# Kernel optimization log

Measured on AMD Instinct MI355X. Metric: run time of the kernel, lower is better.

## Reference

```python
import jax, jax.numpy as jnp
import numpy as np
from jax.ops import segment_sum, segment_max

H, C = 2, 32            # heads, per-head channels (hidden = H*C = 64)
HID = H * C
L = 2                   # num_layers
EPS = 1e-5              # LayerNorm eps
NEG_SLOPE = 0.2         # GATv2 leaky_relu slope
NP_, NA_, E_, DIN, DOUT = 200_000, 100_000, 1_000_000, 128, 64


def setup_inputs() -> dict:
    ks = jax.random.split(jax.random.key(0), 16)
    s = 0.05
    return {
        "x_paper": jax.random.normal(ks[0], (NP_, DIN), jnp.float32),
        "x_author": jax.random.normal(ks[1], (NA_, DIN), jnp.float32),
        "ei_writes_src": jax.random.randint(ks[2], (E_,), 0, NA_),
        "ei_writes_dst": jax.random.randint(ks[3], (E_,), 0, NP_),
        "ei_rev_src": jax.random.randint(ks[4], (E_,), 0, NP_),
        "ei_rev_dst": jax.random.randint(ks[5], (E_,), 0, NA_),
        "ei_cites_src": jax.random.randint(ks[6], (E_,), 0, NP_),
        "ei_cites_dst": jax.random.randint(ks[7], (E_,), 0, NP_),
        "inW_paper": jax.random.normal(ks[8], (DIN, HID)) * s,
        "inW_author": jax.random.normal(ks[9], (DIN, HID)) * s,
        "gat_Wl": jax.random.normal(ks[10], (L, 3, HID, HID)) * s,
        "gat_bl": jnp.zeros((L, 3, HID)),
        "gat_Wr": jax.random.normal(ks[11], (L, 3, HID, HID)) * s,
        "gat_br": jnp.zeros((L, 3, HID)),
        "gat_att": jax.random.normal(ks[12], (L, 3, H, C)) * s,
        "gat_bias": jnp.zeros((L, 3, HID)),
        "ln_scale": jnp.ones((L, 2, HID)),
        "ln_bias": jnp.zeros((L, 2, HID)),
        "outW_paper": jax.random.normal(ks[13], (HID, DOUT)) * s,
        "outb_paper": jnp.zeros((DOUT,)),
        "outW_author": jax.random.normal(ks[14], (HID, DOUT)) * s,
        "outb_author": jnp.zeros((DOUT,)),
    }


def _gatv2(h_src, h_dst, src, dst, Wl, bl, Wr, br, att, bias):
    """PyG GATv2Conv(64, 32, heads=2, concat=True, add_self_loops=False)."""
    nd = h_dst.shape[0]
    xl = (h_src @ Wl + bl).reshape(-1, H, C)           # [Ns,H,C]
    xr = (h_dst @ Wr + br).reshape(-1, H, C)           # [Nd,H,C]
    e = jax.nn.leaky_relu(xl[src] + xr[dst], NEG_SLOPE)  # [E,H,C] gather+add
    logits = jnp.einsum('ehc,hc->eh', e, att)          # [E,H]
    m = jax.lax.stop_gradient(segment_max(logits, dst, num_segments=nd))
    ex = jnp.exp(logits - m[dst])                      # stable segment softmax
    den = segment_sum(ex, dst, num_segments=nd)
    alpha = ex / den[dst]                              # [E,H]
    agg = segment_sum(xl[src] * alpha[..., None], dst, num_segments=nd)
    return agg.reshape(nd, HID) + bias


def _ln(v, g, b):
    mu = v.mean(-1, keepdims=True)
    var = ((v - mu) ** 2).mean(-1, keepdims=True)
    return (v - mu) / jnp.sqrt(var + EPS) * g + b


def _forward(x_paper, x_author, ints, params):
    ws, wd, rs, rd, cs, cd = ints
    (inW_p, inW_a, Wl, bl, Wr, br, att, gbias, lng, lnb,
     oWp, obp, oWa, oba) = params
    h = {"paper": x_paper @ inW_p, "author": x_author @ inW_a}
    rels = [("author", "paper", ws, wd),   # writes
            ("paper", "author", rs, rd),   # rev_writes
            ("paper", "paper", cs, cd)]    # cites
    for l in range(L):
        new = {"paper": 0.0, "author": 0.0}
        for r, (st, dt, src, dst) in enumerate(rels):
            new[dt] = new[dt] + _gatv2(h[st], h[dt], src, dst,
                                       Wl[l, r], bl[l, r], Wr[l, r], br[l, r],
                                       att[l, r], gbias[l, r])
        # HeteroConv(aggr='sum') -> LayerNorm -> ReLU (dropout is eval no-op)
        h = {nt: jax.nn.relu(_ln(new[nt], lng[l, i], lnb[l, i]))
             for i, nt in enumerate(("paper", "author"))}
    out_p = h["paper"] @ oWp + obp
    out_a = h["author"] @ oWa + oba
    return jnp.concatenate([out_p, out_a], axis=0)  # [Np+Na, DOUT]


def reference(x_paper, x_author, ei_writes_src, ei_writes_dst, ei_rev_src,
              ei_rev_dst, ei_cites_src, ei_cites_dst, inW_paper, inW_author,
              gat_Wl, gat_bl, gat_Wr, gat_br, gat_att, gat_bias, ln_scale,
              ln_bias, outW_paper, outb_paper, outW_author, outb_author):
    ints = (ei_writes_src, ei_writes_dst, ei_rev_src, ei_rev_dst,
            ei_cites_src, ei_cites_dst)
    params = (inW_paper, inW_author, gat_Wl, gat_bl, gat_Wr, gat_br, gat_att,
              gat_bias, ln_scale, ln_bias, outW_paper, outb_paper,
              outW_author, outb_author)
    return _forward(x_paper, x_author, ints, params)
```

## Files before the change

### kernel.cpp

```cpp
#include <hip/hip_runtime.h>
#include <hip/hip_bf16.h>


#define NPAPER  200000
#define NAUTHOR 100000
#define NEDGE   1000000

#define NB128_P 1563
#define NB128_A 782
#define NB64_P  3125
#define NB64_A  1563

#define BIN_SHIFT 10
#define BIN_SIZE  1024
#define NBIN_P    196
#define NBIN_A    98
#define NBIN_TOT  (NBIN_P + NBIN_A + NBIN_P)
#define CAP_P     8192
#define CAP_A     16384
#define RELOFF1   (NBIN_P * CAP_P)
#define RELOFF2   (NBIN_P * CAP_P + NBIN_A * CAP_A)
#define BINNED_TOT (NBIN_P * CAP_P + NBIN_A * CAP_A + NBIN_P * CAP_P)
#define EPT       8
#define NBLK_BIN  489

#define LOG2E 1.4426950408889634f

typedef __attribute__((ext_vector_type(8))) short short8;
typedef __attribute__((ext_vector_type(4))) float f32x4;
typedef __attribute__((ext_vector_type(2))) float f32x2;

__device__ inline float b2f(__hip_bfloat16 v) { return __bfloat162float(v); }

__device__ inline short f2bs(float f) {
    unsigned u = __float_as_uint(f);
    u += 0x7FFFu + ((u >> 16) & 1u);
    return (short)(u >> 16);
}

__device__ inline float wireF(const void* p, int i, int f32) {
    return f32 ? ((const float*)p)[i]
               : b2f(((const __hip_bfloat16*)p)[i]);
}

__device__ inline const int* sel3(int r, const int* a, const int* b, const int* c) {
    return r == 0 ? a : (r == 1 ? b : c);
}
__device__ inline int* sel3m(int r, int* a, int* b, int* c) {
    return r == 0 ? a : (r == 1 ? b : c);
}

__device__ inline f32x2 unpack2(unsigned u) {
    f32x2 r;
    r.x = __uint_as_float(u << 16);
    r.y = __uint_as_float(u & 0xFFFF0000u);
    return r;
}

template <int CTRL>
__device__ inline float dpp_add(float v) {
    const int r = __builtin_amdgcn_update_dpp(
        0, __float_as_int(v), CTRL, 0xF, 0xF, true);
    return v + __int_as_float(r);
}
__device__ inline float hs16(float v) {
    v = dpp_add<0x128>(v);
    v = dpp_add<0x124>(v);
    v = dpp_add<0x122>(v);
    v = dpp_add<0x121>(v);
    return v;
}
__device__ inline float sum32(float v) {
    v = hs16(v);
    const int s = __builtin_amdgcn_ds_swizzle(__float_as_int(v), 0x401F);
    return v + __int_as_float(s);
}

__global__ void detect_mode(const unsigned* __restrict__ lns, int* __restrict__ flag) {
    if (threadIdx.x == 0 && blockIdx.x == 0)
        flag[0] = (lns[0] == 0x3F800000u) ? 1 : 0;
}

__global__ __launch_bounds__(256) void gemm_in(
    const void* __restrict__ A0v, const void* __restrict__ B0v,
    void* __restrict__ Y0v, int N0, int nt0, int g0,
    const void* __restrict__ A1v, const void* __restrict__ B1v,
    void* __restrict__ Y1v, int N1, int nt1,
    const int* __restrict__ flagp)
{
    const int f32 = flagp[0];
    constexpr int K = 128, SB = K + 8;
    __shared__ short Bs[64 * SB];

    int bid = blockIdx.x;
    const void* Av; const void* Bv; void* Yv; int N, ntiles, gstep, t0;
    if (bid < g0) {
        Av = A0v; Bv = B0v; Yv = Y0v; N = N0; ntiles = nt0; gstep = g0; t0 = bid;
    } else {
        Av = A1v; Bv = B1v; Yv = Y1v; N = N1; ntiles = nt1;
        gstep = (int)gridDim.x - g0; t0 = bid - g0;
    }

    const int tid = threadIdx.x;
    for (int idx = tid; idx < K * 64; idx += 256) {
        const int k = idx >> 6, n = idx & 63;
        const short v = f32 ? f2bs(((const float*)Bv)[idx])
                            : ((const short*)Bv)[idx];
        Bs[n * SB + k] = v;
    }
    __syncthreads();
    if (t0 >= ntiles) return;

    const int wave = tid >> 6;
    const int lane = tid & 63;
    const int l15  = lane & 15;
    const int quad = lane >> 4;

    for (int t = t0; t < ntiles; t += gstep) {
        const int rowbase = t * 64 + wave * 16;
        int r = rowbase + l15;
        if (r >= N) r = N - 1;

        short8 af[4];
#pragma unroll
        for (int kit = 0; kit < 4; kit++) {
            const int k0 = kit * 32 + quad * 8;
            if (f32) {
                const float* Ar = (const float*)Av + (size_t)r * K + k0;
                const float4 x0 = *reinterpret_cast<const float4*>(Ar);
                const float4 x1 = *reinterpret_cast<const float4*>(Ar + 4);
                short8 tt;
                tt[0] = f2bs(x0.x); tt[1] = f2bs(x0.y);
                tt[2] = f2bs(x0.z); tt[3] = f2bs(x0.w);
                tt[4] = f2bs(x1.x); tt[5] = f2bs(x1.y);
                tt[6] = f2bs(x1.z); tt[7] = f2bs(x1.w);
                af[kit] = tt;
            } else {
                af[kit] = *reinterpret_cast<const short8*>(
                    (const short*)Av + (size_t)r * K + k0);
            }
        }

        f32x4 acc[4] = {};
#pragma unroll
        for (int kit = 0; kit < 4; kit++) {
            const int k0 = kit * 32 + quad * 8;
#pragma unroll
            for (int cg = 0; cg < 4; cg++) {
                const short8 bf = *reinterpret_cast<const short8*>(
                    &Bs[(cg * 16 + l15) * SB + k0]);
                acc[cg] = __builtin_amdgcn_mfma_f32_16x16x32_bf16(
                    af[kit], bf, acc[cg], 0, 0, 0);
            }
        }

#pragma unroll
        for (int cg = 0; cg < 4; cg++) {
            const int col = cg * 16 + l15;
#pragma unroll
            for (int rr = 0; rr < 4; rr++) {
                const int row = rowbase + quad * 4 + rr;
                if (row < N)
                    ((__hip_bfloat16*)Yv)[(size_t)row * 64 + col] =
                        __float2bfloat16(acc[cg][rr]);
            }
        }
    }
}

struct J6 {
    const void* A[6];
    const void* W[6];
    int         woff[6];
    const void* bias[6];
    int         boff[6];
    void*       Y[6];
    int         N[6];
    int         nt[6];
    int         gb[7];
};

__global__ __launch_bounds__(256) void gemm_ps6(J6 j, const int* __restrict__ flagp)
{
    const int f32 = flagp[0];
    constexpr int K = 64, SB = K + 8;
    __shared__ short Bs[64 * SB];
    __shared__ float sbias[64];
    __shared__ __align__(16) char outs[4][4096];

    const int bid = blockIdx.x;
    int jid = 0;
#pragma unroll
    for (int q = 0; q < 5; q++)
        if (bid >= j.gb[q + 1]) jid = q + 1;

    const void* Av = j.A[jid];
    void* Yv = j.Y[jid];
    const int N = j.N[jid];
    const int ntiles = j.nt[jid];
    const int gstep = j.gb[jid + 1] - j.gb[jid];
    const int t0 = bid - j.gb[jid];

    const int tid = threadIdx.x;
    {
        const short* Ws = (const short*)j.W[jid];
        const float* Wf = (const float*)j.W[jid];
        const int wo = j.woff[jid];
        for (int idx = tid; idx < K * 64; idx += 256) {
            const int k = idx >> 6, n = idx & 63;
            const short v = f32 ? f2bs(Wf[wo + idx]) : Ws[wo + idx];
            Bs[n * SB + k] = v;
        }
        if (tid < 64)
            sbias[tid] = wireF(j.bias[jid], j.boff[jid] + tid, f32);
    }
    __syncthreads();
    if (t0 >= ntiles) return;

    const int wave = tid >> 6;
    const int lane = tid & 63;
    const int l15  = lane & 15;
    const int quad = lane >> 4;
    char* const myout = outs[wave];

    short8 a_cur[2][2], a_nxt[2][2];

    auto ldA = [&](int t, short8 (&af)[2][2]) {
        const int rowb = t * 128 + wave * 32;
#pragma unroll
        for (int kit = 0; kit < 2; kit++) {
            const int k0 = kit * 32 + quad * 8;
#pragma unroll
            for (int rg = 0; rg < 2; rg++) {
                int r = rowb + rg * 16 + l15;
                if (r >= N) r = N - 1;
                af[kit][rg] = *reinterpret_cast<const short8*>(
                    (const short*)Av + (size_t)r * K + k0);
            }
        }
    };

    ldA(t0, a_cur);
    for (int t = t0; ; ) {
        const int tn = t + gstep;
        const bool hn = tn < ntiles;
        if (hn) ldA(tn, a_nxt);

        f32x4 acc[2][4] = {};
#pragma unroll
        for (int kit = 0; kit < 2; kit++) {
            const int k0 = kit * 32 + quad * 8;
#pragma unroll
            for (int cg = 0; cg < 4; cg++) {
                const short8 bf = *reinterpret_cast<const short8*>(
                    &Bs[(cg * 16 + l15) * SB + k0]);
#pragma unroll
                for (int rg = 0; rg < 2; rg++)
                    acc[rg][cg] = __builtin_amdgcn_mfma_f32_16x16x32_bf16(
                        a_cur[kit][rg], bf, acc[rg][cg], 0, 0, 0);
            }
        }

        const int rowbase = t * 128 + wave * 32;
#pragma unroll
        for (int rg = 0; rg < 2; rg++)
#pragma unroll
        for (int cg = 0; cg < 4; cg++) {
            const int col = cg * 16 + l15;
            const float bv = sbias[col];
#pragma unroll
            for (int r = 0; r < 4; r++) {
                const int rl = rg * 16 + quad * 4 + r;
                const unsigned a = (unsigned)(rl * 128 + col * 2)
                                 ^ (unsigned)((rl & 7) << 4);
                *reinterpret_cast<short*>(myout + a) =
                    f2bs(acc[rg][cg][r] + bv);
            }
        }
#pragma unroll
        for (int i = 0; i < 4; i++) {
            const unsigned a = i * 1024 + lane * 16;
            const int rl = a >> 7;
            const unsigned as = a ^ (unsigned)((rl & 7) << 4);
            const int grow = rowbase + rl;
            if (grow < N) {
                const uint4 v = *reinterpret_cast<const uint4*>(myout + as);
                *reinterpret_cast<uint4*>(
                    (__hip_bfloat16*)Yv + (size_t)grow * 64 + ((a & 127) >> 1)) = v;
            }
        }

        if (!hn) break;
#pragma unroll
        for (int kit = 0; kit < 2; kit++) {
            a_cur[kit][0] = a_nxt[kit][0];
            a_cur[kit][1] = a_nxt[kit][1];
        }
        t = tn;
    }
}

__global__ __launch_bounds__(256) void gemm_out(
    const void* __restrict__ A0v, const void* __restrict__ B0v,
    const void* __restrict__ bias0v,
    void* __restrict__ Yv, int N0, int row0_off, int nt0, int g0,
    const void* __restrict__ A1v, const void* __restrict__ B1v,
    const void* __restrict__ bias1v, int N1, int row1_off, int nt1,
    const int* __restrict__ flagp)
{
    const int f32 = flagp[0];
    constexpr int K = 64, SB = K + 8;
    __shared__ short Bs[64 * SB];
    __shared__ float sbias[64];
    __shared__ __align__(16) char outs[4][8192];

    int bid = blockIdx.x;
    const void* Av; const void* Bv; const void* biasv;
    int N, row_off, ntiles, gstep, t0;
    if (bid < g0) {
        Av = A0v; Bv = B0v; biasv = bias0v; N = N0; row_off = row0_off;
        ntiles = nt0; gstep = g0; t0 = bid;
    } else {
        Av = A1v; Bv = B1v; biasv = bias1v; N = N1; row_off = row1_off;
        ntiles = nt1; gstep = (int)gridDim.x - g0; t0 = bid - g0;
    }

    const int tid = threadIdx.x;
    for (int idx = tid; idx < K * 64; idx += 256) {
        const int k = idx >> 6, n = idx & 63;
        const short v = f32 ? f2bs(((const float*)Bv)[idx])
                            : ((const short*)Bv)[idx];
        Bs[n * SB + k] = v;
    }
    if (tid < 64) sbias[tid] = wireF(biasv, tid, f32);
    __syncthreads();
    if (t0 >= ntiles) return;

    const int wave = tid >> 6;
    const int lane = tid & 63;
    const int l15  = lane & 15;
    const int quad = lane >> 4;
    char* const myout = outs[wave];

    short8 a_cur[2][2], a_nxt[2][2];
    auto ldA = [&](int t, short8 (&af)[2][2]) {
        const int rowb = t * 128 + wave * 32;
#pragma unroll
        for (int kit = 0; kit < 2; kit++) {
            const int k0 = kit * 32 + quad * 8;
#pragma unroll
            for (int rg = 0; rg < 2; rg++) {
                int r = rowb + rg * 16 + l15;
                if (r >= N) r = N - 1;
                af[kit][rg] = *reinterpret_cast<const short8*>(
                    (const short*)Av + (size_t)r * K + k0);
            }
        }
    };

    ldA(t0, a_cur);
    for (int t = t0; ; ) {
        const int tn = t + gstep;
        const bool hn = tn < ntiles;
        if (hn) ldA(tn, a_nxt);

        f32x4 acc[2][4] = {};
#pragma unroll
        for (int kit = 0; kit < 2; kit++) {
            const int k0 = kit * 32 + quad * 8;
#pragma unroll
            for (int cg = 0; cg < 4; cg++) {
                const short8 bf = *reinterpret_cast<const short8*>(
                    &Bs[(cg * 16 + l15) * SB + k0]);
#pragma unroll
                for (int rg = 0; rg < 2; rg++)
                    acc[rg][cg] = __builtin_amdgcn_mfma_f32_16x16x32_bf16(
                        a_cur[kit][rg], bf, acc[rg][cg], 0, 0, 0);
            }
        }

        const int rowbase = t * 128 + wave * 32;
        if (!f32) {
#pragma unroll
            for (int rg = 0; rg < 2; rg++)
#pragma unroll
            for (int cg = 0; cg < 4; cg++) {
                const int col = cg * 16 + l15;
                const float bv = sbias[col];
#pragma unroll
                for (int r = 0; r < 4; r++) {
                    const int rl = rg * 16 + quad * 4 + r;
                    const unsigned a = (unsigned)(rl * 128 + col * 2)
                                     ^ (unsigned)((rl & 7) << 4);
                    *reinterpret_cast<short*>(myout + a) =
                        f2bs(acc[rg][cg][r] + bv);
                }
            }
#pragma unroll
            for (int i = 0; i < 4; i++) {
                const unsigned a = i * 1024 + lane * 16;
                const int rl = a >> 7;
                const unsigned as = a ^ (unsigned)((rl & 7) << 4);
                const int grow = rowbase + rl;
                if (grow < N) {
                    const uint4 v = *reinterpret_cast<const uint4*>(myout + as);
                    *reinterpret_cast<uint4*>(
                        (__hip_bfloat16*)Yv
                        + (size_t)(grow + row_off) * 64 + ((a & 127) >> 1)) = v;
                }
            }
        } else {
#pragma unroll
            for (int rg = 0; rg < 2; rg++)
#pragma unroll
            for (int cg = 0; cg < 4; cg++) {
                const int col = cg * 16 + l15;
                const float bv = sbias[col];
#pragma unroll
                for (int r = 0; r < 4; r++) {
                    const int rl = rg * 16 + quad * 4 + r;
                    const unsigned a = (unsigned)(rl * 256 + col * 4)
                                     ^ (unsigned)((rl & 15) << 4);
                    *reinterpret_cast<float*>(myout + a) = acc[rg][cg][r] + bv;
                }
            }
#pragma unroll
            for (int i = 0; i < 8; i++) {
                const unsigned a = i * 1024 + lane * 16;
                const int rl = a >> 8;
                const unsigned as = a ^ (unsigned)((rl & 15) << 4);
                const int grow = rowbase + rl;
                if (grow < N) {
                    const float4 v = *reinterpret_cast<const float4*>(myout + as);
                    *reinterpret_cast<float4*>(
                        (float*)Yv
                        + (size_t)(grow + row_off) * 64 + ((a & 255) >> 2)) = v;
                }
            }
        }

        if (!hn) break;
#pragma unroll
        for (int kit = 0; kit < 2; kit++) {
            a_cur[kit][0] = a_nxt[kit][0];
            a_cur[kit][1] = a_nxt[kit][1];
        }
        t = tn;
    }
}

__global__ __launch_bounds__(256) void scatter_pad(
    const int* __restrict__ s0, const int* __restrict__ s1, const int* __restrict__ s2,
    const int* __restrict__ d0, const int* __restrict__ d1, const int* __restrict__ d2,
    int* __restrict__ g_bincnt, unsigned* __restrict__ binned)
{
    int bid = blockIdx.x;
    const int rel = bid / NBLK_BIN;
    bid -= rel * NBLK_BIN;
    const int* src = sel3(rel, s0, s1, s2);
    const int* dst = sel3(rel, d0, d1, d2);
    const int nbin = (rel == 1) ? NBIN_A : NBIN_P;
    const int cap  = (rel == 1) ? CAP_A : CAP_P;
    const int boff = (rel == 0) ? 0 : ((rel == 1) ? NBIN_P : NBIN_P + NBIN_A);
    unsigned* bout = binned + ((rel == 0) ? 0 : ((rel == 1) ? RELOFF1 : RELOFF2));

    __shared__ int lcnt[NBIN_P];
    __shared__ int lbase[NBIN_P];
    for (int i = threadIdx.x; i < nbin; i += 256) lcnt[i] = 0;
    __syncthreads();

    const int e0 = bid * (256 * EPT) + threadIdx.x;
    int mybin[EPT], myslot[EPT];
    unsigned mypack[EPT];
#pragma unroll
    for (int i = 0; i < EPT; i++) {
        const int e = e0 + i * 256;
        if (e < NEDGE) {
            const int D = dst[e];
            const int b = D >> BIN_SHIFT;
            mybin[i]  = b;
            mypack[i] = (unsigned)src[e] | ((unsigned)(D & (BIN_SIZE - 1)) << 18);
            myslot[i] = atomicAdd(&lcnt[b], 1);
        } else mybin[i] = -1;
    }
    __syncthreads();
    for (int i = threadIdx.x; i < nbin; i += 256) {
        const int cn = lcnt[i];
        lbase[i] = cn ? atomicAdd(&g_bincnt[boff + i], cn) : 0;
    }
    __syncthreads();
#pragma unroll
    for (int i = 0; i < EPT; i++)
        if (mybin[i] >= 0) {
            const int pos = lbase[mybin[i]] + myslot[i];
            if (pos < cap)
                bout[(size_t)mybin[i] * cap + pos] = mypack[i];
        }
}

__global__ __launch_bounds__(256) void csr_binscan(
    const int* __restrict__ g_bincnt, int* __restrict__ g_binbase,
    int* __restrict__ rp0, int* __restrict__ rp1, int* __restrict__ rp2)
{
    __shared__ int lds[NBIN_TOT];
    for (int i = threadIdx.x; i < NBIN_TOT; i += 256) lds[i] = g_bincnt[i];
    __syncthreads();
    if (threadIdx.x < 3) {
        const int rel  = threadIdx.x;
        const int nbin = (rel == 1) ? NBIN_A : NBIN_P;
        const int boff = (rel == 0) ? 0 : ((rel == 1) ? NBIN_P : NBIN_P + NBIN_A);
        int run = 0;
        for (int i = 0; i < nbin; i++) {
            const int cn = lds[boff + i];
            lds[boff + i] = run;
            run += cn;
        }
        int* rp = sel3m(rel, rp0, rp1, rp2);
        rp[(rel == 1) ? NAUTHOR : NPAPER] = NEDGE;
    }
    __syncthreads();
    for (int i = threadIdx.x; i < NBIN_TOT; i += 256)
        g_binbase[i] = lds[i];
}

__global__ __launch_bounds__(256) void csr_build(
    const unsigned* __restrict__ binned, const int* __restrict__ g_binbase,
    const int* __restrict__ g_bincnt,
    int* __restrict__ rp0, int* __restrict__ rp1, int* __restrict__ rp2,
    int* __restrict__ c0, int* __restrict__ c1, int* __restrict__ c2)
{
    int bid = blockIdx.x;
    int rel, boff, N, cap;
    const unsigned* bin;
    if (bid < NBIN_P) {
        rel = 0; boff = 0; N = NPAPER; cap = CAP_P;
        bin = binned + (size_t)bid * CAP_P;
    } else if (bid < NBIN_P + NBIN_A) {
        rel = 1; bid -= NBIN_P; boff = NBIN_P; N = NAUTHOR; cap = CAP_A;
        bin = binned + RELOFF1 + (size_t)bid * CAP_A;
    } else {
        rel = 2; bid -= NBIN_P + NBIN_A; boff = NBIN_P + NBIN_A; N = NPAPER; cap = CAP_P;
        bin = binned + RELOFF2 + (size_t)bid * CAP_P;
    }

    const int base = g_binbase[boff + bid];
    int cnt = g_bincnt[boff + bid];
    if (cnt > cap) cnt = cap;
    int* row_ptr = sel3m(rel, rp0, rp1, rp2);
    int* csr     = sel3m(rel, c0, c1, c2);

    __shared__ int off[BIN_SIZE];
    __shared__ int lds[256];
    for (int i = threadIdx.x; i < BIN_SIZE; i += 256) off[i] = 0;
    __syncthreads();
    for (int i = threadIdx.x; i < cnt; i += 256)
        atomicAdd(&off[bin[i] >> 18], 1);
    __syncthreads();

    const int t  = threadIdx.x;
    const int i4 = t * 4;
    const int v0 = off[i4], v1 = off[i4 + 1], v2 = off[i4 + 2], v3 = off[i4 + 3];
    const int tsum = v0 + v1 + v2 + v3;
    lds[t] = tsum;
    __syncthreads();
    for (int o = 1; o < 256; o <<= 1) {
        const int x = (t >= o) ? lds[t - o] : 0;
        __syncthreads();
        lds[t] += x;
        __syncthreads();
    }
    const int run = lds[t] - tsum;
    const int ex0 = run, ex1 = ex0 + v0, ex2 = ex1 + v1, ex3 = ex2 + v2;
    off[i4] = ex0; off[i4 + 1] = ex1; off[i4 + 2] = ex2; off[i4 + 3] = ex3;
    const int d0g = bid * BIN_SIZE + i4;
    if (d0g     < N) row_ptr[d0g]     = base + ex0;
    if (d0g + 1 < N) row_ptr[d0g + 1] = base + ex1;
    if (d0g + 2 < N) row_ptr[d0g + 2] = base + ex2;
    if (d0g + 3 < N) row_ptr[d0g + 3] = base + ex3;
    __syncthreads();

    for (int i = threadIdx.x; i < cnt; i += 256) {
        const unsigned pk = bin[i];
        const int slot = atomicAdd(&off[pk >> 18], 1);
        csr[base + slot] = (int)(pk & 0x3FFFFu);
    }
}

__device__ inline void gat_core_h(
    const int* __restrict__ csr_src, const unsigned* __restrict__ xlw,
    int beg, int end, int hbase, int cp,
    const f32x2 xr2, float a0, float a1,
    float& accx, float& accy, float& den)
{
    const int n = end - beg;
    const int m = (n + 3) >> 2;
    f32x2 acc2 = {0.0f, 0.0f};
    float dn = 0.0f;

    int lidx;
    {
        const int e = beg + cp;
        lidx = csr_src[(e < end) ? e : beg];
    }
    auto loadq = [&](unsigned (&B)[4], int it) {
#pragma unroll
        for (int k = 0; k < 4; k++) {
            const int s = __shfl(lidx, hbase + ((it & 7) << 2) + k, 64);
            B[k] = xlw[(size_t)s * 32 + cp];
        }
    };

    unsigned G[4];
    loadq(G, 0);
    for (int it = 0; ; ) {
        const int nx = it + 1;
        const bool hn = nx < m;
        unsigned H[4];
        if (hn) {
            if ((nx & 7) == 0) {
                const int e = beg + (nx << 2) + cp;
                lidx = csr_src[(e < end) ? e : beg];
            }
            loadq(H, nx);
        }

        f32x2 xv[4];
        float u[4];
#pragma unroll
        for (int k = 0; k < 4; k++) {
            xv[k] = unpack2(G[k]);
            f32x2 t = xv[k] + xr2;
            t = __builtin_elementwise_max(t, 0.2f * t);
            u[k] = fmaf(t.y, a1, t.x * a0);
        }
#pragma unroll
        for (int k = 0; k < 4; k++) u[k] = hs16(u[k]);
#pragma unroll
        for (int k = 0; k < 4; k++) {
            const float e = ((it << 2) + k < n)
                          ? __builtin_amdgcn_exp2f(u[k]) : 0.0f;
            acc2 += e * xv[k];
            dn   += e;
        }

        if (!hn) break;
        G[0] = H[0]; G[1] = H[1]; G[2] = H[2]; G[3] = H[3];
        it = nx;
    }
    accx = acc2.x;
    accy = acc2.y;
    den  = dn;
}

__global__ __launch_bounds__(256) void gat_all(
    const int* __restrict__ rp0, const int* __restrict__ cs0,
    const __hip_bfloat16* __restrict__ xl0, const __hip_bfloat16* __restrict__ xr0,
    const int* __restrict__ rp2, const int* __restrict__ cs2,
    const __hip_bfloat16* __restrict__ xl2, const __hip_bfloat16* __restrict__ xr2,
    const int* __restrict__ rp1, const int* __restrict__ cs1,
    const __hip_bfloat16* __restrict__ xl1, const __hip_bfloat16* __restrict__ xr1,
    const void* __restrict__ att, int ao0, int ao1, int ao2,
    const void* __restrict__ gb, int bo0, int bo1, int bo2,
    const void* __restrict__ lng, int goffP, int goffA,
    const void* __restrict__ lnb, int boffP, int boffA,
    __hip_bfloat16* __restrict__ h_p, __hip_bfloat16* __restrict__ h_a,
    const int* __restrict__ flagp)
{
    const int gnode = blockIdx.x * 8 + (threadIdx.x >> 5);
    const int hbase = threadIdx.x & 32;
    const int cp    = threadIdx.x & 31;
    const int f32   = flagp[0];
    const int c0 = 2 * cp, c1 = 2 * cp + 1;

    float vx, vy;
    int goff, boff;
    __hip_bfloat16* hout; int dout;

    if (gnode < NPAPER) {
        const int d = gnode;
        vx = wireF(gb, bo0 + c0, f32) + wireF(gb, bo2 + c0, f32);
        vy = wireF(gb, bo0 + c1, f32) + wireF(gb, bo2 + c1, f32);

        {
            const int beg = rp0[d], end = rp0[d + 1];
            if (beg != end) {
                const unsigned uxr = ((const unsigned*)xr0)[(size_t)d * 32 + cp];
                float ax, ay, dn;
                gat_core_h(cs0, (const unsigned*)xl0, beg, end, hbase, cp,
                           unpack2(uxr),
                           wireF(att, ao0 + c0, f32) * LOG2E,
                           wireF(att, ao0 + c1, f32) * LOG2E, ax, ay, dn);
                vx += ax / dn; vy += ay / dn;
            }
        }
        {
            const int beg = rp2[d], end = rp2[d + 1];
            if (beg != end) {
                const unsigned uxr = ((const unsigned*)xr2)[(size_t)d * 32 + cp];
                float ax, ay, dn;
                gat_core_h(cs2, (const unsigned*)xl2, beg, end, hbase, cp,
                           unpack2(uxr),
                           wireF(att, ao2 + c0, f32) * LOG2E,
                           wireF(att, ao2 + c1, f32) * LOG2E, ax, ay, dn);
                vx += ax / dn; vy += ay / dn;
            }
        }
        goff = goffP; boff = boffP;
        hout = h_p; dout = d;
    } else {
        const int d = gnode - NPAPER;
        if (d >= NAUTHOR) return;
        vx = wireF(gb, bo1 + c0, f32);
        vy = wireF(gb, bo1 + c1, f32);

        const int beg = rp1[d], end = rp1[d + 1];
        if (beg != end) {
            const unsigned uxr = ((const unsigned*)xr1)[(size_t)d * 32 + cp];
            float ax, ay, dn;
            gat_core_h(cs1, (const unsigned*)xl1, beg, end, hbase, cp,
                       unpack2(uxr),
                       wireF(att, ao1 + c0, f32) * LOG2E,
                       wireF(att, ao1 + c1, f32) * LOG2E, ax, ay, dn);
            vx += ax / dn; vy += ay / dn;
        }
        goff = goffA; boff = boffA;
        hout = h_a; dout = d;
    }

    const float mu = sum32(vx + vy) * (1.0f / 64.0f);
    const float dx = vx - mu, dy = vy - mu;
    const float var = sum32(dx * dx + dy * dy) * (1.0f / 64.0f);
    const float sc = rsqrtf(var + 1e-5f);
    float y0 = dx * sc * wireF(lng, goff + c0, f32) + wireF(lnb, boff + c0, f32);
    float y1 = dy * sc * wireF(lng, goff + c1, f32) + wireF(lnb, boff + c1, f32);
    y0 = (y0 < 0.0f) ? 0.0f : y0;
    y1 = (y1 < 0.0f) ? 0.0f : y1;

    const unsigned u = (unsigned)(unsigned short)f2bs(y0)
                     | ((unsigned)(unsigned short)f2bs(y1) << 16);
    ((unsigned*)hout)[(size_t)dout * 32 + cp] = u;
}

extern "C" void kernel_launch(void* const* d_in, const int* in_sizes, int n_in,
                              void* d_out, int out_size, void* d_ws, size_t ws_size,
                              hipStream_t stream)
{
    const void* x_p   = d_in[0];
    const void* x_a   = d_in[1];
    const int* e_ws_s = (const int*)d_in[2];
    const int* e_ws_d = (const int*)d_in[3];
    const int* e_rv_s = (const int*)d_in[4];
    const int* e_rv_d = (const int*)d_in[5];
    const int* e_ci_s = (const int*)d_in[6];
    const int* e_ci_d = (const int*)d_in[7];
    const void* inW_p = d_in[8];
    const void* inW_a = d_in[9];
    const void* Wl    = d_in[10];
    const void* bl    = d_in[11];
    const void* Wr    = d_in[12];
    const void* br    = d_in[13];
    const void* att   = d_in[14];
    const void* gbias = d_in[15];
    const void* lng   = d_in[16];
    const void* lnb   = d_in[17];
    const void* oWp   = d_in[18];
    const void* obp   = d_in[19];
    const void* oWa   = d_in[20];
    const void* oba   = d_in[21];

    char* p = (char*)d_ws;
    auto carve = [&](size_t bytes) -> char* {
        char* r = p;
        p += (bytes + 255) & ~(size_t)255;
        return r;
    };
    int* flag = (int*)carve(256);
    __hip_bfloat16* h_p = (__hip_bfloat16*)carve((size_t)NPAPER  * 64 * 2);
    __hip_bfloat16* h_a = (__hip_bfloat16*)carve((size_t)NAUTHOR * 64 * 2);
    __hip_bfloat16* xl0 = (__hip_bfloat16*)carve((size_t)NAUTHOR * 64 * 2);
    __hip_bfloat16* xr0 = (__hip_bfloat16*)carve((size_t)NPAPER  * 64 * 2);
    __hip_bfloat16* xl1 = (__hip_bfloat16*)carve((size_t)NPAPER  * 64 * 2);
    __hip_bfloat16* xr1 = (__hip_bfloat16*)carve((size_t)NAUTHOR * 64 * 2);
    __hip_bfloat16* xl2 = (__hip_bfloat16*)carve((size_t)NPAPER  * 64 * 2);
    __hip_bfloat16* xr2 = (__hip_bfloat16*)carve((size_t)NPAPER  * 64 * 2);
    int *csr_src[3], *row_ptr[3];
    for (int r = 0; r < 3; r++) {
        csr_src[r] = (int*)carve((size_t)NEDGE * 4);
        row_ptr[r] = (int*)carve(((size_t)NPAPER + 1) * 4);
    }
    unsigned* binned = (unsigned*)carve((size_t)BINNED_TOT * 4);
    int* g_bincnt  = (int*)carve(NBIN_TOT * 4);
    int* g_binbase = (int*)carve(NBIN_TOT * 4);

    detect_mode<<<dim3(1), dim3(64), 0, stream>>>((const unsigned*)lng, flag);

    (void)hipMemsetAsync(g_bincnt, 0, NBIN_TOT * 4, stream);
    scatter_pad<<<dim3(3 * NBLK_BIN), dim3(256), 0, stream>>>(
        e_ws_s, e_rv_s, e_ci_s, e_ws_d, e_rv_d, e_ci_d, g_bincnt, binned);
    csr_binscan<<<dim3(1), dim3(256), 0, stream>>>(
        g_bincnt, g_binbase, row_ptr[0], row_ptr[1], row_ptr[2]);
    csr_build<<<dim3(NBIN_TOT), dim3(256), 0, stream>>>(
        binned, g_binbase, g_bincnt, row_ptr[0], row_ptr[1], row_ptr[2],
        csr_src[0], csr_src[1], csr_src[2]);

    {
        const int GT = 2048;
        const int g0 = (int)((long long)GT * NB64_P / (NB64_P + NB64_A));
        gemm_in<<<dim3(GT), dim3(256), 0, stream>>>(
            x_p, inW_p, h_p, NPAPER, NB64_P, g0,
            x_a, inW_a, h_a, NAUTHOR, NB64_A, flag);
    }

    for (int l = 0; l < 2; l++) {
        const int wo0 = (l * 3 + 0) * 4096, bo0 = (l * 3 + 0) * 64;
        const int wo1 = (l * 3 + 1) * 4096, bo1 = (l * 3 + 1) * 64;
        const int wo2 = (l * 3 + 2) * 4096, bo2 = (l * 3 + 2) * 64;

        J6 j;
        const void* As[6] = { h_a, h_p, h_p, h_p, h_p, h_a };
        const void* Ws[6] = { Wl,  Wr,  Wl,  Wr,  Wl,  Wr  };
        const int  wos[6] = { wo0, wo0, wo2, wo2, wo1, wo1 };
        const void* Bi[6] = { bl,  br,  bl,  br,  bl,  br  };
        const int  bos[6] = { bo0, bo0, bo2, bo2, bo1, bo1 };
        void*      Ys[6] = { xl0, xr0, xl2, xr2, xl1, xr1 };
        const int  Nsz[6] = { NAUTHOR, NPAPER, NPAPER, NPAPER, NPAPER, NAUTHOR };
        const int  nts[6] = { NB128_A, NB128_P, NB128_P, NB128_P, NB128_P, NB128_A };
        const int GT6 = 1536;
        int total = 0;
        for (int q = 0; q < 6; q++) total += nts[q];
        j.gb[0] = 0;
        for (int q = 0; q < 6; q++) {
            j.A[q] = As[q]; j.W[q] = Ws[q]; j.woff[q] = wos[q];
            j.bias[q] = Bi[q]; j.boff[q] = bos[q];
            j.Y[q] = Ys[q]; j.N[q] = Nsz[q]; j.nt[q] = nts[q];
            int g = (int)((long long)GT6 * nts[q] / total);
            if (g < 1) g = 1;
            j.gb[q + 1] = j.gb[q] + g;
        }
        j.gb[6] = GT6;
        gemm_ps6<<<dim3(GT6), dim3(256), 0, stream>>>(j, flag);

        gat_all<<<dim3((NPAPER + NAUTHOR) / 8), dim3(256), 0, stream>>>(
            row_ptr[0], csr_src[0], xl0, xr0,
            row_ptr[2], csr_src[2], xl2, xr2,
            row_ptr[1], csr_src[1], xl1, xr1,
            att, bo0, bo1, bo2,
            gbias, bo0, bo1, bo2,
            lng, (l * 2 + 0) * 64, (l * 2 + 1) * 64,
            lnb, (l * 2 + 0) * 64, (l * 2 + 1) * 64,
            h_p, h_a, flag);
    }

    {
        const int GT = 768;
        const int g0 = (int)((long long)GT * NB128_P / (NB128_P + NB128_A));
        gemm_out<<<dim3(GT), dim3(256), 0, stream>>>(
            h_p, oWp, obp, d_out, NPAPER, 0, NB128_P, g0,
            h_a, oWa, oba, NAUTHOR, NPAPER, NB128_A, flag);
    }
}
```

Baseline: 724.3 us.

## Process each GAT destination node with 16 lanes of 4 channels

The GAT aggregation kernel now gives each destination node 16 lanes instead of 32, and each lane handles 4 bf16 channels through 8-byte loads. Each 64-lane wave then covers four nodes rather than two, per-head reductions shrink to 8-lane reductions, and the LayerNorm reduction spans 16 lanes. The aim is fewer, wider gather loads and less wasted lane work on low-degree nodes, at the cost of more registers per lane and more serial edge iterations per node.

Result: slower. 746.8 us (+3.1%).

```diff
diff --git a/kernel.cpp b/kernel.cpp
--- a/kernel.cpp
+++ b/kernel.cpp
@@ -70,9 +70,10 @@
     v = dpp_add<0x121>(v);
     return v;
 }
-__device__ inline float sum32(float v) {
-    v = hs16(v);
-    const int s = __builtin_amdgcn_ds_swizzle(__float_as_int(v), 0x401F);
+__device__ inline float hs8(float v) {
+    v = dpp_add<0xB1>(v);
+    v = dpp_add<0x4E>(v);
+    const int s = __builtin_amdgcn_ds_swizzle(__float_as_int(v), 0x101F);
     return v + __int_as_float(s);
 }
 
@@ -586,70 +587,76 @@
     }
 }
 
-__device__ inline void gat_core_h(
-    const int* __restrict__ csr_src, const unsigned* __restrict__ xlw,
-    int beg, int end, int hbase, int cp,
-    const f32x2 xr2, float a0, float a1,
-    float& accx, float& accy, float& den)
+__device__ inline void gat_core_q(
+    const int* __restrict__ csr_src, const uint2* __restrict__ xlw2,
+    int beg, int end, int qbase, int ql,
+    const f32x2 xr01, const f32x2 xr23,
+    const f32x2 a01, const f32x2 a23,
+    f32x2& s01o, f32x2& s23o, float& deno)
 {
     const int n = end - beg;
     const int m = (n + 3) >> 2;
-    f32x2 acc2 = {0.0f, 0.0f};
+    f32x2 s01 = {0.0f, 0.0f}, s23 = {0.0f, 0.0f};
     float dn = 0.0f;
 
     int lidx;
     {
-        const int e = beg + cp;
+        const int e = beg + ql;
         lidx = csr_src[(e < end) ? e : beg];
     }
-    auto loadq = [&](unsigned (&B)[4], int it) {
+    auto loadq = [&](uint2 (&B)[4], int it) {
 #pragma unroll
         for (int k = 0; k < 4; k++) {
-            const int s = __shfl(lidx, hbase + ((it & 7) << 2) + k, 64);
-            B[k] = xlw[(size_t)s * 32 + cp];
+            const int s = __shfl(lidx, qbase + ((it & 3) << 2) + k, 64);
+            B[k] = xlw2[(size_t)s * 16 + ql];
         }
     };
 
-    unsigned G[4];
+    uint2 G[4];
     loadq(G, 0);
     for (int it = 0; ; ) {
         const int nx = it + 1;
         const bool hn = nx < m;
-        unsigned H[4];
+        uint2 H[4];
         if (hn) {
-            if ((nx & 7) == 0) {
-                const int e = beg + (nx << 2) + cp;
+            if ((nx & 3) == 0) {
+                const int e = beg + (nx << 2) + ql;
                 lidx = csr_src[(e < end) ? e : beg];
             }
             loadq(H, nx);
         }
 
-        f32x2 xv[4];
+        f32x2 x01[4], x23[4];
         float u[4];
 #pragma unroll
         for (int k = 0; k < 4; k++) {
-            xv[k] = unpack2(G[k]);
-            f32x2 t = xv[k] + xr2;
-            t = __builtin_elementwise_max(t, 0.2f * t);
-            u[k] = fmaf(t.y, a1, t.x * a0);
-        }
-#pragma unroll
-        for (int k = 0; k < 4; k++) u[k] = hs16(u[k]);
+            x01[k] = unpack2(G[k].x);
+            x23[k] = unpack2(G[k].y);
+            f32x2 t01 = x01[k] + xr01;
+            t01 = __builtin_elementwise_max(t01, 0.2f * t01);
+            f32x2 t23 = x23[k] + xr23;
+            t23 = __builtin_elementwise_max(t23, 0.2f * t23);
+            float v = t01.x * a01.x;
+            v = fmaf(t01.y, a01.y, v);
+            v = fmaf(t23.x, a23.x, v);
+            u[k] = fmaf(t23.y, a23.y, v);
+        }
+#pragma unroll
+        for (int k = 0; k < 4; k++) u[k] = hs8(u[k]);
 #pragma unroll
         for (int k = 0; k < 4; k++) {
             const float e = ((it << 2) + k < n)
                           ? __builtin_amdgcn_exp2f(u[k]) : 0.0f;
-            acc2 += e * xv[k];
-            dn   += e;
+            s01 += e * x01[k];
+            s23 += e * x23[k];
+            dn  += e;
         }
 
         if (!hn) break;
         G[0] = H[0]; G[1] = H[1]; G[2] = H[2]; G[3] = H[3];
         it = nx;
     }
-    accx = acc2.x;
-    accy = acc2.y;
-    den  = dn;
+    s01o = s01; s23o = s23; deno = dn;
 }
 
 __global__ __launch_bounds__(256) void gat_all(
@@ -666,79 +673,104 @@
     __hip_bfloat16* __restrict__ h_p, __hip_bfloat16* __restrict__ h_a,
     const int* __restrict__ flagp)
 {
-    const int gnode = blockIdx.x * 8 + (threadIdx.x >> 5);
-    const int hbase = threadIdx.x & 32;
-    const int cp    = threadIdx.x & 31;
+    const int gnode = blockIdx.x * 16 + (threadIdx.x >> 4);
+    const int qbase = threadIdx.x & 48;
+    const int ql    = threadIdx.x & 15;
     const int f32   = flagp[0];
-    const int c0 = 2 * cp, c1 = 2 * cp + 1;
-
-    float vx, vy;
+    const int c0 = 4 * ql;
+
+    f32x2 v01, v23;
     int goff, boff;
     __hip_bfloat16* hout; int dout;
 
     if (gnode < NPAPER) {
         const int d = gnode;
-        vx = wireF(gb, bo0 + c0, f32) + wireF(gb, bo2 + c0, f32);
-        vy = wireF(gb, bo0 + c1, f32) + wireF(gb, bo2 + c1, f32);
+        v01.x = wireF(gb, bo0 + c0,     f32) + wireF(gb, bo2 + c0,     f32);
+        v01.y = wireF(gb, bo0 + c0 + 1, f32) + wireF(gb, bo2 + c0 + 1, f32);
+        v23.x = wireF(gb, bo0 + c0 + 2, f32) + wireF(gb, bo2 + c0 + 2, f32);
+        v23.y = wireF(gb, bo0 + c0 + 3, f32) + wireF(gb, bo2 + c0 + 3, f32);
 
         {
             const int beg = rp0[d], end = rp0[d + 1];
             if (beg != end) {
-                const unsigned uxr = ((const unsigned*)xr0)[(size_t)d * 32 + cp];
-                float ax, ay, dn;
-                gat_core_h(cs0, (const unsigned*)xl0, beg, end, hbase, cp,
-                           unpack2(uxr),
-                           wireF(att, ao0 + c0, f32) * LOG2E,
-                           wireF(att, ao0 + c1, f32) * LOG2E, ax, ay, dn);
-                vx += ax / dn; vy += ay / dn;
+                const uint2 ux = ((const uint2*)xr0)[(size_t)d * 16 + ql];
+                f32x2 a01, a23;
+                a01.x = wireF(att, ao0 + c0,     f32) * LOG2E;
+                a01.y = wireF(att, ao0 + c0 + 1, f32) * LOG2E;
+                a23.x = wireF(att, ao0 + c0 + 2, f32) * LOG2E;
+                a23.y = wireF(att, ao0 + c0 + 3, f32) * LOG2E;
+                f32x2 s01, s23; float dn;
+                gat_core_q(cs0, (const uint2*)xl0, beg, end, qbase, ql,
+                           unpack2(ux.x), unpack2(ux.y), a01, a23, s01, s23, dn);
+                const float inv = 1.0f / dn;
+                v01 += s01 * inv; v23 += s23 * inv;
             }
         }
         {
             const int beg = rp2[d], end = rp2[d + 1];
             if (beg != end) {
-                const unsigned uxr = ((const unsigned*)xr2)[(size_t)d * 32 + cp];
-                float ax, ay, dn;
-                gat_core_h(cs2, (const unsigned*)xl2, beg, end, hbase, cp,
-                           unpack2(uxr),
-                           wireF(att, ao2 + c0, f32) * LOG2E,
-                           wireF(att, ao2 + c1, f32) * LOG2E, ax, ay, dn);
-                vx += ax / dn; vy += ay / dn;
-            }
-        }
-        goff = goffP; boff = boffP;
-        hout = h_p; dout = d;
+                const uint2 ux = ((const uint2*)xr2)[(size_t)d * 16 + ql];
+                f32x2 a01, a23;
+                a01.x = wireF(att, ao2 + c0,     f32) * LOG2E;
+                a01.y = wireF(att, ao2 + c0 + 1, f32) * LOG2E;
+                a23.x = wireF(att, ao2 + c0 + 2, f32) * LOG2E;
+                a23.y = wireF(att, ao2 + c0 + 3, f32) * LOG2E;
+                f32x2 s01, s23; float dn;
+                gat_core_q(cs2, (const uint2*)xl2, beg, end, qbase, ql,
+                           unpack2(ux.x), unpack2(ux.y), a01, a23, s01, s23, dn);
+                const float inv = 1.0f / dn;
+                v01 += s01 * inv; v23 += s23 * inv;
+            }
+        }
+        goff = goffP; boff = boffP; hout = h_p; dout = d;
     } else {
         const int d = gnode - NPAPER;
         if (d >= NAUTHOR) return;
-        vx = wireF(gb, bo1 + c0, f32);
-        vy = wireF(gb, bo1 + c1, f32);
+        v01.x = wireF(gb, bo1 + c0,     f32);
+        v01.y = wireF(gb, bo1 + c0 + 1, f32);
+        v23.x = wireF(gb, bo1 + c0 + 2, f32);
+        v23.y = wireF(gb, bo1 + c0 + 3, f32);
 
         const int beg = rp1[d], end = rp1[d + 1];
         if (beg != end) {
-            const unsigned uxr = ((const unsigned*)xr1)[(size_t)d * 32 + cp];
-            float ax, ay, dn;
-            gat_core_h(cs1, (const unsigned*)xl1, beg, end, hbase, cp,
-                       unpack2(uxr),
-                       wireF(att, ao1 + c0, f32) * LOG2E,
-                       wireF(att, ao1 + c1, f32) * LOG2E, ax, ay, dn);
-            vx += ax / dn; vy += ay / dn;
-        }
-        goff = goffA; boff = boffA;
-        hout = h_a; dout = d;
-    }
-
-    const float mu = sum32(vx + vy) * (1.0f / 64.0f);
-    const float dx = vx - mu, dy = vy - mu;
-    const float var = sum32(dx * dx + dy * dy) * (1.0f / 64.0f);
+            const uint2 ux = ((const uint2*)xr1)[(size_t)d * 16 + ql];
+            f32x2 a01, a23;
+            a01.x = wireF(att, ao1 + c0,     f32) * LOG2E;
+            a01.y = wireF(att, ao1 + c0 + 1, f32) * LOG2E;
+            a23.x = wireF(att, ao1 + c0 + 2, f32) * LOG2E;
+            a23.y = wireF(att, ao1 + c0 + 3, f32) * LOG2E;
+            f32x2 s01, s23; float dn;
+            gat_core_q(cs1, (const uint2*)xl1, beg, end, qbase, ql,
+                       unpack2(ux.x), unpack2(ux.y), a01, a23, s01, s23, dn);
+            const float inv = 1.0f / dn;
+            v01 += s01 * inv; v23 += s23 * inv;
+        }
+        goff = goffA; boff = boffA; hout = h_a; dout = d;
+    }
+
+    const float s = (v01.x + v01.y) + (v23.x + v23.y);
+    const float mu = hs16(s) * (1.0f / 64.0f);
+    const f32x2 mu2 = {mu, mu};
+    const f32x2 d01 = v01 - mu2, d23 = v23 - mu2;
+    const float q = (d01.x * d01.x + d01.y * d01.y)
+                  + (d23.x * d23.x + d23.y * d23.y);
+    const float var = hs16(q) * (1.0f / 64.0f);
     const float sc = rsqrtf(var + 1e-5f);
-    float y0 = dx * sc * wireF(lng, goff + c0, f32) + wireF(lnb, boff + c0, f32);
-    float y1 = dy * sc * wireF(lng, goff + c1, f32) + wireF(lnb, boff + c1, f32);
+    float y0 = d01.x * sc * wireF(lng, goff + c0,     f32) + wireF(lnb, boff + c0,     f32);
+    float y1 = d01.y * sc * wireF(lng, goff + c0 + 1, f32) + wireF(lnb, boff + c0 + 1, f32);
+    float y2 = d23.x * sc * wireF(lng, goff + c0 + 2, f32) + wireF(lnb, boff + c0 + 2, f32);
+    float y3 = d23.y * sc * wireF(lng, goff + c0 + 3, f32) + wireF(lnb, boff + c0 + 3, f32);
     y0 = (y0 < 0.0f) ? 0.0f : y0;
     y1 = (y1 < 0.0f) ? 0.0f : y1;
-
-    const unsigned u = (unsigned)(unsigned short)f2bs(y0)
-                     | ((unsigned)(unsigned short)f2bs(y1) << 16);
-    ((unsigned*)hout)[(size_t)dout * 32 + cp] = u;
+    y2 = (y2 < 0.0f) ? 0.0f : y2;
+    y3 = (y3 < 0.0f) ? 0.0f : y3;
+
+    uint2 u;
+    u.x = (unsigned)(unsigned short)f2bs(y0)
+        | ((unsigned)(unsigned short)f2bs(y1) << 16);
+    u.y = (unsigned)(unsigned short)f2bs(y2)
+        | ((unsigned)(unsigned short)f2bs(y3) << 16);
+    ((uint2*)hout)[(size_t)dout * 16 + ql] = u;
 }
 
 extern "C" void kernel_launch(void* const* d_in, const int* in_sizes, int n_in,
@@ -840,7 +872,7 @@
         j.gb[6] = GT6;
         gemm_ps6<<<dim3(GT6), dim3(256), 0, stream>>>(j, flag);
 
-        gat_all<<<dim3((NPAPER + NAUTHOR) / 8), dim3(256), 0, stream>>>(
+        gat_all<<<dim3((NPAPER + NAUTHOR) / 16), dim3(256), 0, stream>>>(
             row_ptr[0], csr_src[0], xl0, xr0,
             row_ptr[2], csr_src[2], xl2, xr2,
             row_ptr[1], csr_src[1], xl1, xr1,
```
